# Optimization experiments

Measured on AMD Instinct MI355X. Metric: run time of the kernel, lower is better.

Reference implementation:

```python
import jax, jax.numpy as jnp
import numpy as np
from jax import lax

VOCAB, EMB, HID = 50000, 1024, 1024
H2 = HID // 2            # per-direction LSTM hidden
T = 4096                 # sequence length
NTAGS, START, STOP = 5, 3, 4
NEG = -10000.0


def setup_inputs() -> dict:
    key = jax.random.key(0)
    ks = jax.random.split(key, 16)
    n = lambda i, shape, s=0.05: (jax.random.normal(ks[i], shape) * s).astype(jnp.float32)
    inp = {
        "sentence": jax.random.randint(ks[0], (T,), 0, VOCAB, dtype=jnp.int64 if jax.config.jax_enable_x64 else jnp.int32),
        "h0": jax.random.normal(ks[1], (2, H2), jnp.float32),
        "c0": jax.random.normal(ks[2], (2, H2), jnp.float32),
        "embed": jax.random.normal(ks[3], (VOCAB, EMB), jnp.float32),
        "Wih_f": n(4, (4 * H2, EMB)), "Whh_f": n(5, (4 * H2, H2)),
        "bih_f": n(6, (4 * H2,)),     "bhh_f": n(7, (4 * H2,)),
        "Wih_b": n(8, (4 * H2, EMB)), "Whh_b": n(9, (4 * H2, H2)),
        "bih_b": n(10, (4 * H2,)),    "bhh_b": n(11, (4 * H2,)),
        "Wout": n(12, (NTAGS, HID)),  "bout": n(13, (NTAGS,)),
    }
    trans = jax.random.normal(ks[14], (NTAGS, NTAGS), jnp.float32)
    trans = trans.at[START, :].set(NEG).at[:, STOP].set(NEG)
    inp["trans"] = trans
    return inp


def _lstm_dir(xs, h0, c0, Wih, Whh, bih, bhh):
    # torch LSTM gate order: i, f, g, o
    def step(carry, x):
        h, c = carry
        g = Wih @ x + bih + Whh @ h + bhh
        i, f, gg, o = jnp.split(g, 4)
        c = jax.nn.sigmoid(f) * c + jax.nn.sigmoid(i) * jnp.tanh(gg)
        h = jax.nn.sigmoid(o) * jnp.tanh(c)
        return (h, c), h
    _, hs = lax.scan(step, (h0, c0), xs)
    return hs  # [T, H2]


def reference(sentence, h0, c0, embed,
              Wih_f, Whh_f, bih_f, bhh_f,
              Wih_b, Whh_b, bih_b, bhh_b,
              Wout, bout, trans):
    xs = embed[sentence]  # [T, EMB]
    hf = _lstm_dir(xs, h0[0], c0[0], Wih_f, Whh_f, bih_f, bhh_f)
    hb = _lstm_dir(xs[::-1], h0[1], c0[1], Wih_b, Whh_b, bih_b, bhh_b)[::-1]
    feats = jnp.concatenate([hf, hb], axis=-1) @ Wout.T + bout  # [T, NTAGS]

    # Viterbi decode
    fv0 = jnp.full((NTAGS,), NEG, jnp.float32).at[START].set(0.0)

    def vstep(fv, feat):
        scores = fv[None, :] + trans            # [next_tag, prev_tag]
        bp = jnp.argmax(scores, axis=1)         # best prev for each next
        fv_new = jnp.max(scores, axis=1) + feat
        return fv_new, bp

    fv, bptrs = lax.scan(vstep, fv0, feats)     # bptrs: [T, NTAGS]
    terminal = fv + trans[STOP]
    best = jnp.argmax(terminal)
    path_score = terminal[best]

    def back(tag, bp):
        prev = bp[tag]
        return prev, prev
    _, path_rev = lax.scan(back, best, bptrs[::-1])  # tags at t=T-1..0, last is START
    full = jnp.concatenate([best[None], path_rev])    # length T+1
    best_path = full[::-1][1:]                        # drop START, forward order, length T
    return path_score, best_path
```

## Files before the change

### kernel.cpp

```cpp
#include <hip/hip_runtime.h>
#include <math.h>
#include <stddef.h>

#define VOCAB 50000
#define EMB   1024
#define H2    512
#define R4    2048
#define TLEN  4096
#define NTAGS 5
#define STARTT 3
#define STOPT  4
#define NEGV  (-10000.0f)

#define DWG   32
#define SLICE 16

typedef unsigned long long u64;

#define ASTORE64(p,v) __hip_atomic_store((p), (v), __ATOMIC_RELAXED, __HIP_MEMORY_SCOPE_AGENT)

__device__ __forceinline__ float fsig(float x) {
    return __builtin_amdgcn_rcpf(1.f + __expf(-x));
}
__device__ __forceinline__ float ftanh(float x) {
    return 1.f - 2.f * __builtin_amdgcn_rcpf(1.f + __expf(2.f * x));
}

__device__ __forceinline__ void spin64(const u64* p, unsigned want,
    unsigned& h0, unsigned& h1, unsigned& h2, unsigned& h3,
    unsigned& h4, unsigned& h5, unsigned& h6, unsigned& h7)
{
    asm volatile(
        "s_waitcnt vmcnt(0)\n\t"
        "global_load_dwordx4 v[32:35], %[p], off sc1\n\t"
        "global_load_dwordx4 v[36:39], %[p], off offset:16 sc1\n\t"
        "global_load_dwordx4 v[40:43], %[p], off offset:32 sc1\n\t"
        "global_load_dwordx4 v[44:47], %[p], off offset:48 sc1\n\t"
        "s_sleep 1\n\t"
        "global_load_dwordx4 v[48:51], %[p], off sc1\n\t"
        "global_load_dwordx4 v[52:55], %[p], off offset:16 sc1\n\t"
        "global_load_dwordx4 v[56:59], %[p], off offset:32 sc1\n\t"
        "global_load_dwordx4 v[60:63], %[p], off offset:48 sc1\n\t"
        "1:\n\t"
        "s_waitcnt vmcnt(4)\n\t"
        "v_cmp_eq_u32 vcc, %[w], v33\n\t"
        "v_cmp_eq_u32 s[20:21], %[w], v35\n\t"
        "s_and_b64 vcc, vcc, s[20:21]\n\t"
        "v_cmp_eq_u32 s[20:21], %[w], v37\n\t"
        "s_and_b64 vcc, vcc, s[20:21]\n\t"
        "v_cmp_eq_u32 s[20:21], %[w], v39\n\t"
        "s_and_b64 vcc, vcc, s[20:21]\n\t"
        "v_cmp_eq_u32 s[20:21], %[w], v41\n\t"
        "s_and_b64 vcc, vcc, s[20:21]\n\t"
        "v_cmp_eq_u32 s[20:21], %[w], v43\n\t"
        "s_and_b64 vcc, vcc, s[20:21]\n\t"
        "v_cmp_eq_u32 s[20:21], %[w], v45\n\t"
        "s_and_b64 vcc, vcc, s[20:21]\n\t"
        "v_cmp_eq_u32 s[20:21], %[w], v47\n\t"
        "s_and_b64 vcc, vcc, s[20:21]\n\t"
        "s_andn2_b64 s[20:21], exec, vcc\n\t"
        "s_cbranch_scc0 3f\n\t"
        "global_load_dwordx4 v[32:35], %[p], off sc1\n\t"
        "global_load_dwordx4 v[36:39], %[p], off offset:16 sc1\n\t"
        "global_load_dwordx4 v[40:43], %[p], off offset:32 sc1\n\t"
        "global_load_dwordx4 v[44:47], %[p], off offset:48 sc1\n\t"
        "s_sleep 1\n\t"
        "s_waitcnt vmcnt(4)\n\t"
        "v_cmp_eq_u32 vcc, %[w], v49\n\t"
        "v_cmp_eq_u32 s[20:21], %[w], v51\n\t"
        "s_and_b64 vcc, vcc, s[20:21]\n\t"
        "v_cmp_eq_u32 s[20:21], %[w], v53\n\t"
        "s_and_b64 vcc, vcc, s[20:21]\n\t"
        "v_cmp_eq_u32 s[20:21], %[w], v55\n\t"
        "s_and_b64 vcc, vcc, s[20:21]\n\t"
        "v_cmp_eq_u32 s[20:21], %[w], v57\n\t"
        "s_and_b64 vcc, vcc, s[20:21]\n\t"
        "v_cmp_eq_u32 s[20:21], %[w], v59\n\t"
        "s_and_b64 vcc, vcc, s[20:21]\n\t"
        "v_cmp_eq_u32 s[20:21], %[w], v61\n\t"
        "s_and_b64 vcc, vcc, s[20:21]\n\t"
        "v_cmp_eq_u32 s[20:21], %[w], v63\n\t"
        "s_and_b64 vcc, vcc, s[20:21]\n\t"
        "s_andn2_b64 s[20:21], exec, vcc\n\t"
        "s_cbranch_scc0 4f\n\t"
        "global_load_dwordx4 v[48:51], %[p], off sc1\n\t"
        "global_load_dwordx4 v[52:55], %[p], off offset:16 sc1\n\t"
        "global_load_dwordx4 v[56:59], %[p], off offset:32 sc1\n\t"
        "global_load_dwordx4 v[60:63], %[p], off offset:48 sc1\n\t"
        "s_sleep 1\n\t"
        "s_branch 1b\n\t"
        "4:\n\t"
        "v_mov_b32 %[h0], v48\n\t"
        "v_mov_b32 %[h1], v50\n\t"
        "v_mov_b32 %[h2], v52\n\t"
        "v_mov_b32 %[h3], v54\n\t"
        "v_mov_b32 %[h4], v56\n\t"
        "v_mov_b32 %[h5], v58\n\t"
        "v_mov_b32 %[h6], v60\n\t"
        "v_mov_b32 %[h7], v62\n\t"
        "s_branch 5f\n\t"
        "3:\n\t"
        "v_mov_b32 %[h0], v32\n\t"
        "v_mov_b32 %[h1], v34\n\t"
        "v_mov_b32 %[h2], v36\n\t"
        "v_mov_b32 %[h3], v38\n\t"
        "v_mov_b32 %[h4], v40\n\t"
        "v_mov_b32 %[h5], v42\n\t"
        "v_mov_b32 %[h6], v44\n\t"
        "v_mov_b32 %[h7], v46\n\t"
        "5:\n\t"
        : [h0]"=v"(h0), [h1]"=v"(h1), [h2]"=v"(h2), [h3]"=v"(h3),
          [h4]"=v"(h4), [h5]"=v"(h5), [h6]"=v"(h6), [h7]"=v"(h7)
        : [p]"v"(p), [w]"v"(want)
        : "v32","v33","v34","v35","v36","v37","v38","v39",
          "v40","v41","v42","v43","v44","v45","v46","v47",
          "v48","v49","v50","v51","v52","v53","v54","v55",
          "v56","v57","v58","v59","v60","v61","v62","v63",
          "s20","s21","vcc","memory");
}

__global__ __launch_bounds__(256) void input_gemm(
    const int* __restrict__ sent, const float* __restrict__ embed,
    const float* __restrict__ WihF, const float* __restrict__ WihB,
    const float* __restrict__ bihF, const float* __restrict__ bhhF,
    const float* __restrict__ bihB, const float* __restrict__ bhhB,
    float* __restrict__ G)
{
    __shared__ float As[32 * 64];
    __shared__ float Bs[32 * 64];
    const int tid = threadIdx.x;
    const int tm = blockIdx.x * 64;
    const int tn = blockIdx.y * 64;
    const int dir = blockIdx.z;
    const float* Wih = dir ? WihB : WihF;

    const int lr = tid >> 2;
    const int lp = tid & 3;
    const int srow = sent[tm + lr];
    const float* arow = embed + (size_t)srow * EMB;
    const float* brow = Wih + (size_t)(tn + lr) * EMB;

    const int mt = (tid & 15) * 4;
    const int nt = (tid >> 4) * 4;
    float acc[4][4] = {};

    for (int k0 = 0; k0 < EMB; k0 += 32) {
        float4 a0 = *(const float4*)(arow + k0 + lp * 8);
        float4 a1 = *(const float4*)(arow + k0 + lp * 8 + 4);
        float4 b0 = *(const float4*)(brow + k0 + lp * 8);
        float4 b1 = *(const float4*)(brow + k0 + lp * 8 + 4);
        __syncthreads();
        const int kb = lp * 8;
        As[(kb + 0) * 64 + lr] = a0.x; As[(kb + 1) * 64 + lr] = a0.y;
        As[(kb + 2) * 64 + lr] = a0.z; As[(kb + 3) * 64 + lr] = a0.w;
        As[(kb + 4) * 64 + lr] = a1.x; As[(kb + 5) * 64 + lr] = a1.y;
        As[(kb + 6) * 64 + lr] = a1.z; As[(kb + 7) * 64 + lr] = a1.w;
        Bs[(kb + 0) * 64 + lr] = b0.x; Bs[(kb + 1) * 64 + lr] = b0.y;
        Bs[(kb + 2) * 64 + lr] = b0.z; Bs[(kb + 3) * 64 + lr] = b0.w;
        Bs[(kb + 4) * 64 + lr] = b1.x; Bs[(kb + 5) * 64 + lr] = b1.y;
        Bs[(kb + 6) * 64 + lr] = b1.z; Bs[(kb + 7) * 64 + lr] = b1.w;
        __syncthreads();
        #pragma unroll
        for (int k = 0; k < 32; ++k) {
            float4 av = *(const float4*)(As + k * 64 + mt);
            float4 bv = *(const float4*)(Bs + k * 64 + nt);
            acc[0][0] += av.x * bv.x; acc[0][1] += av.x * bv.y; acc[0][2] += av.x * bv.z; acc[0][3] += av.x * bv.w;
            acc[1][0] += av.y * bv.x; acc[1][1] += av.y * bv.y; acc[1][2] += av.y * bv.z; acc[1][3] += av.y * bv.w;
            acc[2][0] += av.z * bv.x; acc[2][1] += av.z * bv.y; acc[2][2] += av.z * bv.z; acc[2][3] += av.z * bv.w;
            acc[3][0] += av.w * bv.x; acc[3][1] += av.w * bv.y; acc[3][2] += av.w * bv.z; acc[3][3] += av.w * bv.w;
        }
    }

    const float* bih = dir ? bihB : bihF;
    const float* bhh = dir ? bhhB : bhhF;
    float4 bias;
    bias.x = bih[tn + nt + 0] + bhh[tn + nt + 0];
    bias.y = bih[tn + nt + 1] + bhh[tn + nt + 1];
    bias.z = bih[tn + nt + 2] + bhh[tn + nt + 2];
    bias.w = bih[tn + nt + 3] + bhh[tn + nt + 3];
    float* Gd = G + (size_t)dir * TLEN * R4;
    #pragma unroll
    for (int ii = 0; ii < 4; ++ii) {
        float4 o;
        o.x = acc[ii][0] + bias.x; o.y = acc[ii][1] + bias.y;
        o.z = acc[ii][2] + bias.z; o.w = acc[ii][3] + bias.w;
        *(float4*)(Gd + (size_t)(tm + mt + ii) * R4 + tn + nt) = o;
    }
}

__global__ __launch_bounds__(512, 1) void lstm_rec(
    const float* __restrict__ WhhF, const float* __restrict__ WhhB,
    const float* __restrict__ h0, const float* __restrict__ c0,
    const float* __restrict__ G, float* __restrict__ hs,
    u64* hbuf)
{
    const int tid  = threadIdx.x;
    const int dir  = blockIdx.x >> 5;
    const int wg   = blockIdx.x & 31;
    const int base = wg * SLICE;
    const int wave = tid >> 6;
    const int wl   = tid & 63;
    const int half = wl >> 5;
    const int gp   = (wl >> 4) & 1;
    const int qs   = wl & 15;
    const int e    = wave * 2 + half;
    const int grow0 = gp * H2 + base + e;
    const int grow1 = (gp + 2) * H2 + base + e;
    const bool prod = (wl & 31) == 0;
    const float* Whh = dir ? WhhB : WhhF;

    float4 W0[8], W1[8];
    {
        const float4* s0 = (const float4*)(Whh + (size_t)grow0 * H2 + qs * 32);
        const float4* s1 = (const float4*)(Whh + (size_t)grow1 * H2 + qs * 32);
        #pragma unroll
        for (int j = 0; j < 8; ++j) { W0[j] = s0[j]; W1[j] = s1[j]; }
    }

    __shared__ float hsh[2][8 * 68];

    u64* hb = hbuf + (size_t)dir * 2 * H2;
    float cc = 0.f;
    if (prod) {
        cc = c0[dir * H2 + base + e];
        float hv = h0[dir * H2 + base + e];
        u64 pack = ((u64)1u << 32) | (u64)__float_as_uint(hv);
        ASTORE64(hb + base + e, pack);
    }

    const float* Gd = G + (size_t)dir * TLEN * R4;
    float* hsd = hs + (size_t)dir * TLEN * H2;
    const ptrdiff_t sstep = dir ? -(ptrdiff_t)R4 : (ptrdiff_t)R4;
    const float* g0p = Gd + (size_t)(dir ? TLEN - 1 : 0) * R4;

    const u64* pollP0 = hb + wl * 8;
    const u64* pollP1 = hb + H2 + wl * 8;

    float gE0 = g0p[grow0], gE1 = g0p[grow1];
    float gO0 = (g0p + sstep)[grow0], gO1 = (g0p + sstep)[grow1];

#define STEP(S, PAR, GR0, GR1)                                                \
  {                                                                           \
    if (wave == 0) {                                                          \
        unsigned x0, x1, x2, x3, x4, x5, x6, x7;                              \
        spin64((PAR) ? pollP1 : pollP0, (unsigned)((S) + 1),                  \
               x0, x1, x2, x3, x4, x5, x6, x7);                               \
        float* dst = &hsh[PAR][(wl >> 3) * 68 + (wl & 7) * 8];                \
        dst[0] = __uint_as_float(x0); dst[1] = __uint_as_float(x1);           \
        dst[2] = __uint_as_float(x2); dst[3] = __uint_as_float(x3);           \
        dst[4] = __uint_as_float(x4); dst[5] = __uint_as_float(x5);           \
        dst[6] = __uint_as_float(x6); dst[7] = __uint_as_float(x7);           \
    }                                                                         \
    __syncthreads();                                                          \
    const float gc0 = GR0, gc1 = GR1;                       \
    {    \
          \
        const int sn = ((S) + 2 < TLEN) ? (S) + 2 : TLEN - 1;                 \
        const float* gn = g0p + (ptrdiff_t)sn * sstep;                        \
        GR0 = gn[grow0]; GR1 = gn[grow1];                                     \
    }                                                                         \
    const float4* hq = (const float4*)(&hsh[PAR][(qs >> 1) * 68 + (qs & 1) * 32]); \
    float p00 = 0.f, p01 = 0.f, p02 = 0.f, p03 = 0.f;                         \
    float p10 = 0.f, p11 = 0.f, p12 = 0.f, p13 = 0.f;                         \
    _Pragma("unroll")                                                         \
    for (int j = 0; j < 8; ++j) {                                             \
        float4 h4 = hq[j];                                                    \
        p00 += W0[j].x * h4.x; p01 += W0[j].y * h4.y;                         \
        p02 += W0[j].z * h4.z; p03 += W0[j].w * h4.w;                         \
        p10 += W1[j].x * h4.x; p11 += W1[j].y * h4.y;                         \
        p12 += W1[j].z * h4.z; p13 += W1[j].w * h4.w;                         \
    }                                                                         \
    float t0 = (p00 + p01) + (p02 + p03);                                     \
    float t1 = (p10 + p11) + (p12 + p13);                                     \
    t0 += __shfl_xor(t0, 1); t0 += __shfl_xor(t0, 2);                         \
    t0 += __shfl_xor(t0, 4); t0 += __shfl_xor(t0, 8);                         \
    t1 += __shfl_xor(t1, 1); t1 += __shfl_xor(t1, 2);                         \
    t1 += __shfl_xor(t1, 4); t1 += __shfl_xor(t1, 8);                         \
    t0 += gc0;                               \
    t1 += gc1;                                                                \
    float pf = __shfl_xor(t0, 16);            \
    float po = __shfl_xor(t1, 16);                            \
    if (prod) {                          \
        float i_ = fsig(t0);                                                  \
        float f_ = fsig(pf);                                                  \
        float g_ = ftanh(t1);                                                 \
        float o_ = fsig(po);                                                  \
        cc = f_ * cc + i_ * g_;                                               \
        float hn = o_ * ftanh(cc);                                            \
        u64 pack = ((u64)(unsigned)((S) + 2) << 32) | (u64)__float_as_uint(hn); \
        ASTORE64(hb + (1 - (PAR)) * H2 + base + e, pack);                     \
        hsd[(size_t)(dir ? (TLEN - 1 - (S)) : (S)) * H2 + base + e] = hn;     \
    }                                                                         \
       \
       \
  }

    for (int s = 0; s < TLEN; s += 2) {
        STEP(s,     0, gE0, gE1);
        STEP(s + 1, 1, gO0, gO1);
    }
#undef STEP
}

__global__ __launch_bounds__(64) void feat_kernel(
    const float* __restrict__ hs, const float* __restrict__ Wout,
    const float* __restrict__ bout, float* __restrict__ feats)
{
    const int t = blockIdx.x;
    const int lane = threadIdx.x;
    const float* hf = hs + (size_t)t * H2;
    const float* hb = hs + (size_t)TLEN * H2 + (size_t)t * H2;
    float x[16];
    #pragma unroll
    for (int r = 0; r < 8; ++r) x[r] = hf[lane + r * 64];
    #pragma unroll
    for (int r = 0; r < 8; ++r) x[8 + r] = hb[lane + r * 64];
    for (int j = 0; j < NTAGS; ++j) {
        const float* wr = Wout + (size_t)j * EMB;
        float p = 0.f;
        #pragma unroll
        for (int r = 0; r < 8; ++r) p += x[r] * wr[lane + r * 64];
        #pragma unroll
        for (int r = 0; r < 8; ++r) p += x[8 + r] * wr[H2 + lane + r * 64];
        #pragma unroll
        for (int off = 32; off > 0; off >>= 1) p += __shfl_down(p, off);
        if (lane == 0) feats[t * NTAGS + j] = p + bout[j];
    }
}

__global__ __launch_bounds__(64) void viterbi_kernel(
    const float* __restrict__ feats, const float* __restrict__ trans,
    float* __restrict__ out)
{
    __shared__ unsigned bp[TLEN];
    __shared__ float fch[256 * NTAGS];
    const int lane = threadIdx.x;
    const bool act = lane < 25;
    const int j = act ? (lane / 5) : 0;
    const int i = act ? (lane % 5) : 0;
    const int j5 = j * 5;
    const float tji = act ? trans[j * 5 + i] : -1e30f;
    float fv = (i == STARTT) ? 0.f : NEGV;

    for (int c0 = 0; c0 < TLEN; c0 += 256) {
        __syncthreads();
        for (int m = lane; m < 256 * NTAGS; m += 64) fch[m] = feats[c0 * NTAGS + m];
        __syncthreads();
        for (int tt = 0; tt < 256; ++tt) {
            float score = fv + tji;
            float v0 = __shfl(score, j5 + 0);
            float v1 = __shfl(score, j5 + 1);
            float v2 = __shfl(score, j5 + 2);
            float v3 = __shfl(score, j5 + 3);
            float v4 = __shfl(score, j5 + 4);
            float mm = v0; int mi = 0;
            if (v1 > mm) { mm = v1; mi = 1; }
            if (v2 > mm) { mm = v2; mi = 2; }
            if (v3 > mm) { mm = v3; mi = 3; }
            if (v4 > mm) { mm = v4; mi = 4; }
            float fnew = mm + fch[tt * NTAGS + j];
            unsigned word = ((unsigned)__shfl(mi, 0)  & 7u)
                          | (((unsigned)__shfl(mi, 5)  & 7u) << 3)
                          | (((unsigned)__shfl(mi, 10) & 7u) << 6)
                          | (((unsigned)__shfl(mi, 15) & 7u) << 9)
                          | (((unsigned)__shfl(mi, 20) & 7u) << 12);
            if (lane == 0) bp[c0 + tt] = word;
            fv = __shfl(fnew, i * 5);
        }
    }
    __syncthreads();

    float tstop = (lane < 5) ? trans[STOPT * 5 + lane] : -1e30f;
    float term = fv + tstop;
    float b0 = __shfl(term, 0), b1 = __shfl(term, 1), b2 = __shfl(term, 2);
    float b3 = __shfl(term, 3), b4 = __shfl(term, 4);
    float bsc = b0; int best = 0;
    if (b1 > bsc) { bsc = b1; best = 1; }
    if (b2 > bsc) { bsc = b2; best = 2; }
    if (b3 > bsc) { bsc = b3; best = 3; }
    if (b4 > bsc) { bsc = b4; best = 4; }

    if (lane == 0) {
        out[0] = bsc;
        int tag = best;
        out[TLEN] = (float)tag;
        #pragma unroll 16
        for (int t = TLEN - 1; t >= 1; --t) {
            tag = (int)((bp[t] >> (3 * tag)) & 7u);
            out[t] = (float)tag;
        }
    }
}

extern "C" void kernel_launch(void* const* d_in, const int* in_sizes, int n_in,
                              void* d_out, int out_size, void* d_ws, size_t ws_size,
                              hipStream_t stream) {
    const int*   sent  = (const int*)d_in[0];
    const float* h0    = (const float*)d_in[1];
    const float* c0    = (const float*)d_in[2];
    const float* embed = (const float*)d_in[3];
    const float* Wih_f = (const float*)d_in[4];
    const float* Whh_f = (const float*)d_in[5];
    const float* bih_f = (const float*)d_in[6];
    const float* bhh_f = (const float*)d_in[7];
    const float* Wih_b = (const float*)d_in[8];
    const float* Whh_b = (const float*)d_in[9];
    const float* bih_b = (const float*)d_in[10];
    const float* bhh_b = (const float*)d_in[11];
    const float* Wout  = (const float*)d_in[12];
    const float* bout  = (const float*)d_in[13];
    const float* trans = (const float*)d_in[14];

    char* ws = (char*)d_ws;
    float*    G     = (float*)(ws);
    float*    hs    = (float*)(ws + 67108864);
    u64*      hbuf  = (u64*)(ws + 83886080);
    float*    feats = (float*)(ws + 83918848);

    hipMemsetAsync(hbuf, 0, 2 * 2 * H2 * sizeof(u64), stream);

    input_gemm<<<dim3(TLEN / 64, R4 / 64, 2), 256, 0, stream>>>(
        sent, embed, Wih_f, Wih_b, bih_f, bhh_f, bih_b, bhh_b, G);
    lstm_rec<<<2 * DWG, 512, 0, stream>>>(Whh_f, Whh_b, h0, c0, G, hs, hbuf);
    feat_kernel<<<TLEN, 64, 0, stream>>>(hs, Wout, bout, feats);
    viterbi_kernel<<<1, 64, 0, stream>>>(feats, trans, (float*)d_out);
}
```

Measured before the change: 7.881 ms.

## Enlarge input GEMM tiles, trim spin-poll sleeps, lighten recurrent-step barrier

The input projection GEMM now uses 128x128 tiles with an 8x8 per-thread micro-tile and a 16-deep k-slice, which raises arithmetic intensity and cuts redundant global and LDS traffic. The spin-poll loop loses its leading vmcnt wait and two of its s_sleep instructions, so it re-polls more aggressively. The per-step __syncthreads is replaced with an explicit lgkmcnt wait plus raw s_barrier and a sched_barrier, and hidden-state writes to LDS become float4 stores. The recurrent weights are pinned in registers through empty asm constraints. Tradeoffs are more register pressure in the GEMM and recurrent kernels, fewer GEMM blocks, and more memory traffic from the tighter polling.

New measurement: 11.49 ms. 1.46x slower.

```diff
diff --git a/kernel.cpp b/kernel.cpp
--- a/kernel.cpp
+++ b/kernel.cpp
@@ -31,7 +31,6 @@
     unsigned& h4, unsigned& h5, unsigned& h6, unsigned& h7)
 {
     asm volatile(
-        "s_waitcnt vmcnt(0)\n\t"
         "global_load_dwordx4 v[32:35], %[p], off sc1\n\t"
         "global_load_dwordx4 v[36:39], %[p], off offset:16 sc1\n\t"
         "global_load_dwordx4 v[40:43], %[p], off offset:32 sc1\n\t"
@@ -64,7 +63,6 @@
         "global_load_dwordx4 v[36:39], %[p], off offset:16 sc1\n\t"
         "global_load_dwordx4 v[40:43], %[p], off offset:32 sc1\n\t"
         "global_load_dwordx4 v[44:47], %[p], off offset:48 sc1\n\t"
-        "s_sleep 1\n\t"
         "s_waitcnt vmcnt(4)\n\t"
         "v_cmp_eq_u32 vcc, %[w], v49\n\t"
         "v_cmp_eq_u32 s[20:21], %[w], v51\n\t"
@@ -87,7 +85,6 @@
         "global_load_dwordx4 v[52:55], %[p], off offset:16 sc1\n\t"
         "global_load_dwordx4 v[56:59], %[p], off offset:32 sc1\n\t"
         "global_load_dwordx4 v[60:63], %[p], off offset:48 sc1\n\t"
-        "s_sleep 1\n\t"
         "s_branch 1b\n\t"
         "4:\n\t"
         "v_mov_b32 %[h0], v48\n\t"
@@ -126,65 +123,71 @@
     const float* __restrict__ bihB, const float* __restrict__ bhhB,
     float* __restrict__ G)
 {
-    __shared__ float As[32 * 64];
-    __shared__ float Bs[32 * 64];
+    __shared__ float As[16][128];
+    __shared__ float Bs[16][128];
     const int tid = threadIdx.x;
-    const int tm = blockIdx.x * 64;
-    const int tn = blockIdx.y * 64;
+    const int tm = blockIdx.x * 128;
+    const int tn = blockIdx.y * 128;
     const int dir = blockIdx.z;
     const float* Wih = dir ? WihB : WihF;
 
-    const int lr = tid >> 2;
-    const int lp = tid & 3;
+    const int lr = tid >> 1;
+    const int lp = (tid & 1) * 8;
     const int srow = sent[tm + lr];
-    const float* arow = embed + (size_t)srow * EMB;
-    const float* brow = Wih + (size_t)(tn + lr) * EMB;
-
-    const int mt = (tid & 15) * 4;
-    const int nt = (tid >> 4) * 4;
-    float acc[4][4] = {};
-
-    for (int k0 = 0; k0 < EMB; k0 += 32) {
-        float4 a0 = *(const float4*)(arow + k0 + lp * 8);
-        float4 a1 = *(const float4*)(arow + k0 + lp * 8 + 4);
-        float4 b0 = *(const float4*)(brow + k0 + lp * 8);
-        float4 b1 = *(const float4*)(brow + k0 + lp * 8 + 4);
+    const float* arow = embed + (size_t)srow * EMB + lp;
+    const float* brow = Wih + (size_t)(tn + lr) * EMB + lp;
+
+    const int mt = (tid & 15) * 8;
+    const int nt = (tid >> 4) * 8;
+    float acc[8][8] = {};
+
+    for (int k0 = 0; k0 < EMB; k0 += 16) {
+        float4 a0 = *(const float4*)(arow + k0);
+        float4 a1 = *(const float4*)(arow + k0 + 4);
+        float4 b0 = *(const float4*)(brow + k0);
+        float4 b1 = *(const float4*)(brow + k0 + 4);
         __syncthreads();
-        const int kb = lp * 8;
-        As[(kb + 0) * 64 + lr] = a0.x; As[(kb + 1) * 64 + lr] = a0.y;
-        As[(kb + 2) * 64 + lr] = a0.z; As[(kb + 3) * 64 + lr] = a0.w;
-        As[(kb + 4) * 64 + lr] = a1.x; As[(kb + 5) * 64 + lr] = a1.y;
-        As[(kb + 6) * 64 + lr] = a1.z; As[(kb + 7) * 64 + lr] = a1.w;
-        Bs[(kb + 0) * 64 + lr] = b0.x; Bs[(kb + 1) * 64 + lr] = b0.y;
-        Bs[(kb + 2) * 64 + lr] = b0.z; Bs[(kb + 3) * 64 + lr] = b0.w;
-        Bs[(kb + 4) * 64 + lr] = b1.x; Bs[(kb + 5) * 64 + lr] = b1.y;
-        Bs[(kb + 6) * 64 + lr] = b1.z; Bs[(kb + 7) * 64 + lr] = b1.w;
+        As[lp + 0][lr] = a0.x; As[lp + 1][lr] = a0.y;
+        As[lp + 2][lr] = a0.z; As[lp + 3][lr] = a0.w;
+        As[lp + 4][lr] = a1.x; As[lp + 5][lr] = a1.y;
+        As[lp + 6][lr] = a1.z; As[lp + 7][lr] = a1.w;
+        Bs[lp + 0][lr] = b0.x; Bs[lp + 1][lr] = b0.y;
+        Bs[lp + 2][lr] = b0.z; Bs[lp + 3][lr] = b0.w;
+        Bs[lp + 4][lr] = b1.x; Bs[lp + 5][lr] = b1.y;
+        Bs[lp + 6][lr] = b1.z; Bs[lp + 7][lr] = b1.w;
         __syncthreads();
         #pragma unroll
-        for (int k = 0; k < 32; ++k) {
-            float4 av = *(const float4*)(As + k * 64 + mt);
-            float4 bv = *(const float4*)(Bs + k * 64 + nt);
-            acc[0][0] += av.x * bv.x; acc[0][1] += av.x * bv.y; acc[0][2] += av.x * bv.z; acc[0][3] += av.x * bv.w;
-            acc[1][0] += av.y * bv.x; acc[1][1] += av.y * bv.y; acc[1][2] += av.y * bv.z; acc[1][3] += av.y * bv.w;
-            acc[2][0] += av.z * bv.x; acc[2][1] += av.z * bv.y; acc[2][2] += av.z * bv.z; acc[2][3] += av.z * bv.w;
-            acc[3][0] += av.w * bv.x; acc[3][1] += av.w * bv.y; acc[3][2] += av.w * bv.z; acc[3][3] += av.w * bv.w;
+        for (int k = 0; k < 16; ++k) {
+            float4 av0 = *(const float4*)(&As[k][mt]);
+            float4 av1 = *(const float4*)(&As[k][mt + 4]);
+            float4 bv0 = *(const float4*)(&Bs[k][nt]);
+            float4 bv1 = *(const float4*)(&Bs[k][nt + 4]);
+            float am[8] = {av0.x, av0.y, av0.z, av0.w, av1.x, av1.y, av1.z, av1.w};
+            float bb[8] = {bv0.x, bv0.y, bv0.z, bv0.w, bv1.x, bv1.y, bv1.z, bv1.w};
+            #pragma unroll
+            for (int i = 0; i < 8; ++i) {
+                #pragma unroll
+                for (int j = 0; j < 8; ++j) acc[i][j] += am[i] * bb[j];
+            }
         }
     }
 
     const float* bih = dir ? bihB : bihF;
     const float* bhh = dir ? bhhB : bhhF;
-    float4 bias;
-    bias.x = bih[tn + nt + 0] + bhh[tn + nt + 0];
-    bias.y = bih[tn + nt + 1] + bhh[tn + nt + 1];
-    bias.z = bih[tn + nt + 2] + bhh[tn + nt + 2];
-    bias.w = bih[tn + nt + 3] + bhh[tn + nt + 3];
+    float bias[8];
+    #pragma unroll
+    for (int j = 0; j < 8; ++j) bias[j] = bih[tn + nt + j] + bhh[tn + nt + j];
     float* Gd = G + (size_t)dir * TLEN * R4;
     #pragma unroll
-    for (int ii = 0; ii < 4; ++ii) {
-        float4 o;
-        o.x = acc[ii][0] + bias.x; o.y = acc[ii][1] + bias.y;
-        o.z = acc[ii][2] + bias.z; o.w = acc[ii][3] + bias.w;
-        *(float4*)(Gd + (size_t)(tm + mt + ii) * R4 + tn + nt) = o;
+    for (int i = 0; i < 8; ++i) {
+        float4 o0, o1;
+        o0.x = acc[i][0] + bias[0]; o0.y = acc[i][1] + bias[1];
+        o0.z = acc[i][2] + bias[2]; o0.w = acc[i][3] + bias[3];
+        o1.x = acc[i][4] + bias[4]; o1.y = acc[i][5] + bias[5];
+        o1.z = acc[i][6] + bias[6]; o1.w = acc[i][7] + bias[7];
+        float* orow = Gd + (size_t)(tm + mt + i) * R4 + tn + nt;
+        *(float4*)(orow) = o0;
+        *(float4*)(orow + 4) = o1;
     }
 }
 
@@ -209,12 +212,20 @@
     const bool prod = (wl & 31) == 0;
     const float* Whh = dir ? WhhB : WhhF;
 
-    float4 W0[8], W1[8];
+    float W0s[32], W1s[32];
     {
         const float4* s0 = (const float4*)(Whh + (size_t)grow0 * H2 + qs * 32);
         const float4* s1 = (const float4*)(Whh + (size_t)grow1 * H2 + qs * 32);
         #pragma unroll
-        for (int j = 0; j < 8; ++j) { W0[j] = s0[j]; W1[j] = s1[j]; }
+        for (int j = 0; j < 8; ++j) {
+            float4 a = s0[j], b = s1[j];
+            W0s[4*j+0] = a.x; W0s[4*j+1] = a.y; W0s[4*j+2] = a.z; W0s[4*j+3] = a.w;
+            W1s[4*j+0] = b.x; W1s[4*j+1] = b.y; W1s[4*j+2] = b.z; W1s[4*j+3] = b.w;
+        }
+        #pragma unroll
+        for (int j = 0; j < 32; ++j) {
+            asm volatile("" : "+v"(W0s[j]), "+v"(W1s[j]));
+        }
     }
 
     __shared__ float hsh[2][8 * 68];
@@ -245,16 +256,21 @@
         unsigned x0, x1, x2, x3, x4, x5, x6, x7;                              \
         spin64((PAR) ? pollP1 : pollP0, (unsigned)((S) + 1),                  \
                x0, x1, x2, x3, x4, x5, x6, x7);                               \
-        float* dst = &hsh[PAR][(wl >> 3) * 68 + (wl & 7) * 8];                \
-        dst[0] = __uint_as_float(x0); dst[1] = __uint_as_float(x1);           \
-        dst[2] = __uint_as_float(x2); dst[3] = __uint_as_float(x3);           \
-        dst[4] = __uint_as_float(x4); dst[5] = __uint_as_float(x5);           \
-        dst[6] = __uint_as_float(x6); dst[7] = __uint_as_float(x7);           \
+        float4 f0, f1;                                                        \
+        f0.x = __uint_as_float(x0); f0.y = __uint_as_float(x1);               \
+        f0.z = __uint_as_float(x2); f0.w = __uint_as_float(x3);               \
+        f1.x = __uint_as_float(x4); f1.y = __uint_as_float(x5);               \
+        f1.z = __uint_as_float(x6); f1.w = __uint_as_float(x7);               \
+        float4* dst = (float4*)&hsh[PAR][(wl >> 3) * 68 + (wl & 7) * 8];      \
+        dst[0] = f0; dst[1] = f1;                                             \
     }                                                                         \
-    __syncthreads();                                                          \
+       \
+       \
+    asm volatile("s_waitcnt lgkmcnt(0)" ::: "memory");                        \
+    __builtin_amdgcn_s_barrier();                                             \
+    __builtin_amdgcn_sched_barrier(0);      \
     const float gc0 = GR0, gc1 = GR1;                       \
     {    \
-          \
         const int sn = ((S) + 2 < TLEN) ? (S) + 2 : TLEN - 1;                 \
         const float* gn = g0p + (ptrdiff_t)sn * sstep;                        \
         GR0 = gn[grow0]; GR1 = gn[grow1];                                     \
@@ -265,10 +281,10 @@
     _Pragma("unroll")                                                         \
     for (int j = 0; j < 8; ++j) {                                             \
         float4 h4 = hq[j];                                                    \
-        p00 += W0[j].x * h4.x; p01 += W0[j].y * h4.y;                         \
-        p02 += W0[j].z * h4.z; p03 += W0[j].w * h4.w;                         \
-        p10 += W1[j].x * h4.x; p11 += W1[j].y * h4.y;                         \
-        p12 += W1[j].z * h4.z; p13 += W1[j].w * h4.w;                         \
+        p00 += W0s[4*j+0] * h4.x; p01 += W0s[4*j+1] * h4.y;                   \
+        p02 += W0s[4*j+2] * h4.z; p03 += W0s[4*j+3] * h4.w;                   \
+        p10 += W1s[4*j+0] * h4.x; p11 += W1s[4*j+1] * h4.y;                   \
+        p12 += W1s[4*j+2] * h4.z; p13 += W1s[4*j+3] * h4.w;                   \
     }                                                                         \
     float t0 = (p00 + p01) + (p02 + p03);                                     \
     float t1 = (p10 + p11) + (p12 + p13);                                     \
@@ -419,7 +435,7 @@
 
     hipMemsetAsync(hbuf, 0, 2 * 2 * H2 * sizeof(u64), stream);
 
-    input_gemm<<<dim3(TLEN / 64, R4 / 64, 2), 256, 0, stream>>>(
+    input_gemm<<<dim3(TLEN / 128, R4 / 128, 2), 256, 0, stream>>>(
         sent, embed, Wih_f, Wih_b, bih_f, bhh_f, bih_b, bhh_b, G);
     lstm_rec<<<2 * DWG, 512, 0, stream>>>(Whh_f, Whh_b, h0, c0, G, hs, hbuf);
     feat_kernel<<<TLEN, 64, 0, stream>>>(hs, Wout, bout, feats);
```
